# Performance work log

Measured on AMD Instinct MI355X. Metric: run time of the kernel, lower is better.

## Reference

```python
import jax, jax.numpy as jnp
import numpy as np

N, E = 50000, 800000
IN_D, HID, H1, OUT_D, H2, EDGE_D = 64, 16, 8, 64, 2, 1
NEG_SLOPE = 0.2


def gatv2_layer(x, src, dst, edge_attr, Wl, Wr, We, att, bias, concat):
    """PyG GATv2Conv (add_self_loops=False, share_weights=False), eval mode (no dropout)."""
    n = x.shape[0]
    H, C = att.shape
    xl = (x @ Wl).reshape(n, H, C)            # source transform
    xr = (x @ Wr).reshape(n, H, C)            # target transform
    ee = (edge_attr @ We).reshape(-1, H, C)   # edge embedding
    z = jax.nn.leaky_relu(xl[src] + xr[dst] + ee, NEG_SLOPE)  # [E,H,C]
    score = jnp.einsum('ehc,hc->eh', z, att)                  # [E,H]
    # softmax over incoming edges per target node
    m = jax.ops.segment_max(score, dst, num_segments=n)
    m = jnp.where(jnp.isfinite(m), m, 0.0)
    a = jnp.exp(score - m[dst])
    denom = jax.ops.segment_sum(a, dst, num_segments=n)
    alpha = a / (denom[dst] + 1e-16)                          # [E,H]
    msg = xl[src] * alpha[..., None]                          # [E,H,C]
    out = jax.ops.segment_sum(msg, dst, num_segments=n)       # [N,H,C]
    if concat:
        return out.reshape(n, H * C) + bias
    return out.mean(axis=1) + bias


def layer_norm(x, g, b):
    mu = x.mean(-1, keepdims=True)
    var = ((x - mu) ** 2).mean(-1, keepdims=True)
    return (x - mu) * jax.lax.rsqrt(var + 1e-5) * g + b


def setup_inputs() -> dict:
    key = jax.random.key(0)
    ks = jax.random.split(key, 24)
    def w(k, *shape):
        fan_in = shape[0]
        return jax.random.normal(k, shape, dtype=jnp.float32) * (1.0 / np.sqrt(fan_in))
    inp = {
        'x': jax.random.normal(ks[0], (N, IN_D), dtype=jnp.float32),
        'edge_index': jax.random.randint(ks[1], (2, E), 0, N, dtype=jnp.int64),
        'edge_attr': jax.random.normal(ks[2], (E, EDGE_D), dtype=jnp.float32),
        # layer 1 (heads=8, out=16, concat)
        'w1_l': w(ks[3], IN_D, H1 * HID), 'w1_r': w(ks[4], IN_D, H1 * HID),
        'w1_e': w(ks[5], EDGE_D, H1 * HID),
        'att1': jax.random.normal(ks[6], (H1, HID), dtype=jnp.float32) * 0.1,
        'b1': jnp.zeros((H1 * HID,), dtype=jnp.float32),
        # layer 2 (heads=2, out=64, mean)
        'w2_l': w(ks[7], H1 * HID, H2 * OUT_D), 'w2_r': w(ks[8], H1 * HID, H2 * OUT_D),
        'w2_e': w(ks[9], EDGE_D, H2 * OUT_D),
        'att2': jax.random.normal(ks[10], (H2, OUT_D), dtype=jnp.float32) * 0.1,
        'b2': jnp.zeros((OUT_D,), dtype=jnp.float32),
        # classifier: Linear + LayerNorm + GELU + ResidualBlockv2
        'wc': w(ks[11], OUT_D, OUT_D), 'bc': jnp.zeros((OUT_D,), dtype=jnp.float32),
        'ln_g': jnp.ones((OUT_D,), dtype=jnp.float32), 'ln_b': jnp.zeros((OUT_D,), dtype=jnp.float32),
        'wr': w(ks[12], OUT_D, OUT_D), 'br': jnp.zeros((OUT_D,), dtype=jnp.float32),
        'lnr_g': jnp.ones((OUT_D,), dtype=jnp.float32), 'lnr_b': jnp.zeros((OUT_D,), dtype=jnp.float32),
    }
    return inp


def reference(x, edge_index, edge_attr, w1_l, w1_r, w1_e, att1, b1,
              w2_l, w2_r, w2_e, att2, b2, wc, bc, ln_g, ln_b, wr, br, lnr_g, lnr_b):
    src, dst = edge_index[0], edge_index[1]
    h = jax.nn.relu(gatv2_layer(x, src, dst, edge_attr, w1_l, w1_r, w1_e, att1, b1, True))
    h = jax.nn.relu(gatv2_layer(h, src, dst, edge_attr, w2_l, w2_r, w2_e, att2, b2, False))
    h = jax.nn.gelu(layer_norm(h @ wc + bc, ln_g, ln_b), approximate=False)
    # ResidualBlockv2: Linear -> LayerNorm -> GELU with residual skip
    h = h + jax.nn.gelu(layer_norm(h @ wr + br, lnr_g, lnr_b), approximate=False)
    return h
```

## Files before the change

### kernel.cpp

```cpp
#include <hip/hip_runtime.h>
#include <math.h>

#define NNODE 50000
#define NEDGE 800000
#define NBLK 196

__device__ __forceinline__ float wsum64(float v) {
    #pragma unroll
    for (int m = 32; m >= 1; m >>= 1) v += __shfl_xor(v, m, 64);
    return v;
}

__device__ __forceinline__ float gelu_exact(float x) {
    return 0.5f * x * (1.0f + erff(x * 0.70710678118654752f));
}

__device__ __forceinline__ float lrelu(float z) { return z > 0.f ? z : 0.2f * z; }

__global__ void fill_u32(unsigned* __restrict__ p, unsigned v, int n) {
    int i = blockIdx.x * blockDim.x + threadIdx.x;
    if (i < n) p[i] = v;
}

__global__ __launch_bounds__(256) void build_deg(const int* __restrict__ ei, int* __restrict__ deg) {
    int e = blockIdx.x * 256 + threadIdx.x;
    if (e >= NEDGE) return;
    atomicAdd(&deg[ei[NEDGE + e]], 1);
}

__global__ __launch_bounds__(256) void scan1(const int* __restrict__ deg,
                                             int* __restrict__ partial,
                                             int* __restrict__ bsum) {
    __shared__ int tmp[256];
    int t = threadIdx.x;
    int gid = blockIdx.x * 256 + t;
    int v = (gid < NNODE) ? deg[gid] : 0;
    tmp[t] = v;
    __syncthreads();
    #pragma unroll
    for (int off = 1; off < 256; off <<= 1) {
        int u = (t >= off) ? tmp[t - off] : 0;
        __syncthreads();
        tmp[t] += u;
        __syncthreads();
    }
    if (gid < NNODE) partial[gid] = tmp[t] - v;
    if (t == 255) bsum[blockIdx.x] = tmp[255];
}

__global__ __launch_bounds__(256) void scan2(int* __restrict__ bsum, int* __restrict__ boff) {
    __shared__ int tmp[256];
    int t = threadIdx.x;
    int v = (t < NBLK) ? bsum[t] : 0;
    tmp[t] = v;
    __syncthreads();
    #pragma unroll
    for (int off = 1; off < 256; off <<= 1) {
        int u = (t >= off) ? tmp[t - off] : 0;
        __syncthreads();
        tmp[t] += u;
        __syncthreads();
    }
    if (t < NBLK) boff[t] = tmp[t] - v;
}

__global__ __launch_bounds__(256) void scan3(const int* __restrict__ partial,
                                             const int* __restrict__ boff,
                                             int* __restrict__ base,
                                             int* __restrict__ cursor) {
    int gid = blockIdx.x * 256 + threadIdx.x;
    if (gid < NNODE) {
        int b = partial[gid] + boff[blockIdx.x];
        base[gid] = b;
        cursor[gid] = b;
    }
    if (gid == 0) base[NNODE] = NEDGE;
}

__global__ __launch_bounds__(256) void scatter_edges(const int* __restrict__ ei,
                                                     const float* __restrict__ ea,
                                                     int* __restrict__ cursor,
                                                     int2* __restrict__ se) {
    int e = blockIdx.x * 256 + threadIdx.x;
    if (e >= NEDGE) return;
    int d = ei[NEDGE + e];
    int i = atomicAdd(&cursor[d], 1);
    se[i] = make_int2(ei[e], __float_as_int(ea[e]));
}

template<int K>
__global__ __launch_bounds__(256) void node_xform(const float* __restrict__ in,
                                                  const float* __restrict__ wl,
                                                  const float* __restrict__ wr,
                                                  float* __restrict__ xl,
                                                  float* __restrict__ xr) {
    __shared__ float xrow[32][K];
    int t = threadIdx.x;
    int n0 = blockIdx.x * 32;
    for (int idx = t; idx < 32 * (K / 4); idx += 256) {
        int row = idx / (K / 4), c4 = idx % (K / 4);
        float4 v = make_float4(0.f, 0.f, 0.f, 0.f);
        if (n0 + row < NNODE) v = ((const float4*)(in + (size_t)(n0 + row) * K))[c4];
        ((float4*)xrow[row])[c4] = v;
    }
    __syncthreads();
    int cg = t & 63, ns = t >> 6;
    const float* wsel = (cg < 32) ? wl : wr;
    float* osel = (cg < 32) ? xl : xr;
    int ccol = (cg & 31) * 4;
    const float* wp = wsel + ccol;
    const float* xbase = xrow[ns * 8];
    float4 acc[8];
    #pragma unroll
    for (int k = 0; k < 8; ++k) acc[k] = make_float4(0.f, 0.f, 0.f, 0.f);
    for (int i = 0; i < K; i += 4) {
        float4 w0 = *(const float4*)(wp + (size_t)(i + 0) * 128);
        float4 w1 = *(const float4*)(wp + (size_t)(i + 1) * 128);
        float4 w2 = *(const float4*)(wp + (size_t)(i + 2) * 128);
        float4 w3 = *(const float4*)(wp + (size_t)(i + 3) * 128);
        #pragma unroll
        for (int k = 0; k < 8; ++k) {
            float4 xv = *(const float4*)(xbase + (size_t)k * K + i);
            acc[k].x += xv.x * w0.x + xv.y * w1.x + xv.z * w2.x + xv.w * w3.x;
            acc[k].y += xv.x * w0.y + xv.y * w1.y + xv.z * w2.y + xv.w * w3.y;
            acc[k].z += xv.x * w0.z + xv.y * w1.z + xv.z * w2.z + xv.w * w3.z;
            acc[k].w += xv.x * w0.w + xv.y * w1.w + xv.z * w2.w + xv.w * w3.w;
        }
    }
    #pragma unroll
    for (int k = 0; k < 8; ++k) {
        int n = n0 + ns * 8 + k;
        if (n < NNODE) *(float4*)(osel + (size_t)n * 128 + ccol) = acc[k];
    }
}

__global__ __launch_bounds__(256) void fused1(const int* __restrict__ base,
                                              const int2* __restrict__ se,
                                              const float* __restrict__ xl,
                                              const float* __restrict__ xr,
                                              const float* __restrict__ w1e,
                                              const float* __restrict__ att1,
                                              const float* __restrict__ b1,
                                              float* __restrict__ h1) {
    int t = threadIdx.x;
    int wv = t >> 6, ln = t & 63;
    int half = ln >> 5, sub = ln & 31;
    int n = blockIdx.x * 4 + wv;
    int ch = sub * 4;
    float4 xrv = *(const float4*)(xr + (size_t)n * 128 + ch);
    float4 wev = *(const float4*)(w1e + ch);
    float4 atv = *(const float4*)(att1 + ch);
    int i0 = base[n], i1 = base[n + 1];
    float m = -1e30f, den = 0.f;
    float4 o = make_float4(0.f, 0.f, 0.f, 0.f);
    int i = i0 + half;
    if (i < i1) {
        int2 r = se[i];
        float4 xv = *(const float4*)(xl + (size_t)r.x * 128 + ch);
        float a = __int_as_float(r.y);
        for (i += 2; i < i1; i += 2) {
            int2 rn = se[i];
            float4 nxv = *(const float4*)(xl + (size_t)rn.x * 128 + ch);
            float na = __int_as_float(rn.y);
            float part = lrelu(fmaf(a, wev.x, xv.x + xrv.x)) * atv.x
                       + lrelu(fmaf(a, wev.y, xv.y + xrv.y)) * atv.y
                       + lrelu(fmaf(a, wev.z, xv.z + xrv.z)) * atv.z
                       + lrelu(fmaf(a, wev.w, xv.w + xrv.w)) * atv.w;
            part += __shfl_xor(part, 1, 64);
            part += __shfl_xor(part, 2, 64);
            float mn = fmaxf(m, part);
            float sc = __expf(m - mn);
            float p  = __expf(part - mn);
            den = den * sc + p;
            o.x = o.x * sc + p * xv.x;
            o.y = o.y * sc + p * xv.y;
            o.z = o.z * sc + p * xv.z;
            o.w = o.w * sc + p * xv.w;
            m = mn;
            xv = nxv; a = na;
        }
        float part = lrelu(fmaf(a, wev.x, xv.x + xrv.x)) * atv.x
                   + lrelu(fmaf(a, wev.y, xv.y + xrv.y)) * atv.y
                   + lrelu(fmaf(a, wev.z, xv.z + xrv.z)) * atv.z
                   + lrelu(fmaf(a, wev.w, xv.w + xrv.w)) * atv.w;
        part += __shfl_xor(part, 1, 64);
        part += __shfl_xor(part, 2, 64);
        float mn = fmaxf(m, part);
        float sc = __expf(m - mn);
        float p  = __expf(part - mn);
        den = den * sc + p;
        o.x = o.x * sc + p * xv.x;
        o.y = o.y * sc + p * xv.y;
        o.z = o.z * sc + p * xv.z;
        o.w = o.w * sc + p * xv.w;
        m = mn;
    }
    float m2   = __shfl_xor(m, 32, 64);
    float den2 = __shfl_xor(den, 32, 64);
    float4 o2;
    o2.x = __shfl_xor(o.x, 32, 64);
    o2.y = __shfl_xor(o.y, 32, 64);
    o2.z = __shfl_xor(o.z, 32, 64);
    o2.w = __shfl_xor(o.w, 32, 64);
    float mn = fmaxf(m, m2);
    float s1 = __expf(m - mn), s2 = __expf(m2 - mn);
    den = den * s1 + den2 * s2;
    float inv = 1.f / (den + 1e-16f);
    if (half == 0) {
        float4 bv = *(const float4*)(b1 + ch);
        float4 res;
        res.x = fmaxf((o.x * s1 + o2.x * s2) * inv + bv.x, 0.f);
        res.y = fmaxf((o.y * s1 + o2.y * s2) * inv + bv.y, 0.f);
        res.z = fmaxf((o.z * s1 + o2.z * s2) * inv + bv.z, 0.f);
        res.w = fmaxf((o.w * s1 + o2.w * s2) * inv + bv.w, 0.f);
        *(float4*)(h1 + (size_t)n * 128 + ch) = res;
    }
}

__global__ __launch_bounds__(256) void fused2cls(const int* __restrict__ base,
                                                 const int2* __restrict__ se,
                                                 const float* __restrict__ xl,
                                                 const float* __restrict__ xr,
                                                 const float* __restrict__ w2e,
                                                 const float* __restrict__ att2,
                                                 const float* __restrict__ b2,
                                                 const float* __restrict__ wc,
                                                 const float* __restrict__ bc,
                                                 const float* __restrict__ lng,
                                                 const float* __restrict__ lnb,
                                                 const float* __restrict__ wrr,
                                                 const float* __restrict__ brr,
                                                 const float* __restrict__ lrg,
                                                 const float* __restrict__ lrb,
                                                 float* __restrict__ out) {
    __shared__ float rowH[4][64];
    __shared__ float rowB[4][64];
    int t = threadIdx.x;
    int wv = t >> 6, ln = t & 63;
    int half = ln >> 5, sub = ln & 31;
    int n = blockIdx.x * 4 + wv;
    int ch = sub * 4;
    float4 xrv = *(const float4*)(xr + (size_t)n * 128 + ch);
    float4 wev = *(const float4*)(w2e + ch);
    float4 atv = *(const float4*)(att2 + ch);
    int i0 = base[n], i1 = base[n + 1];
    float m = -1e30f, den = 0.f;
    float4 o = make_float4(0.f, 0.f, 0.f, 0.f);
    int i = i0 + half;
    if (i < i1) {
        int2 r = se[i];
        float4 xv = *(const float4*)(xl + (size_t)r.x * 128 + ch);
        float a = __int_as_float(r.y);
        for (i += 2; i < i1; i += 2) {
            int2 rn = se[i];
            float4 nxv = *(const float4*)(xl + (size_t)rn.x * 128 + ch);
            float na = __int_as_float(rn.y);
            float part = lrelu(fmaf(a, wev.x, xv.x + xrv.x)) * atv.x
                       + lrelu(fmaf(a, wev.y, xv.y + xrv.y)) * atv.y
                       + lrelu(fmaf(a, wev.z, xv.z + xrv.z)) * atv.z
                       + lrelu(fmaf(a, wev.w, xv.w + xrv.w)) * atv.w;
            part += __shfl_xor(part, 1, 64);
            part += __shfl_xor(part, 2, 64);
            part += __shfl_xor(part, 4, 64);
            part += __shfl_xor(part, 8, 64);
            float mn = fmaxf(m, part);
            float sc = __expf(m - mn);
            float p  = __expf(part - mn);
            den = den * sc + p;
            o.x = o.x * sc + p * xv.x;
            o.y = o.y * sc + p * xv.y;
            o.z = o.z * sc + p * xv.z;
            o.w = o.w * sc + p * xv.w;
            m = mn;
            xv = nxv; a = na;
        }
        float part = lrelu(fmaf(a, wev.x, xv.x + xrv.x)) * atv.x
                   + lrelu(fmaf(a, wev.y, xv.y + xrv.y)) * atv.y
                   + lrelu(fmaf(a, wev.z, xv.z + xrv.z)) * atv.z
                   + lrelu(fmaf(a, wev.w, xv.w + xrv.w)) * atv.w;
        part += __shfl_xor(part, 1, 64);
        part += __shfl_xor(part, 2, 64);
        part += __shfl_xor(part, 4, 64);
        part += __shfl_xor(part, 8, 64);
        float mn = fmaxf(m, part);
        float sc = __expf(m - mn);
        float p  = __expf(part - mn);
        den = den * sc + p;
        o.x = o.x * sc + p * xv.x;
        o.y = o.y * sc + p * xv.y;
        o.z = o.z * sc + p * xv.z;
        o.w = o.w * sc + p * xv.w;
        m = mn;
    }
    float m2   = __shfl_xor(m, 32, 64);
    float den2 = __shfl_xor(den, 32, 64);
    float4 o2;
    o2.x = __shfl_xor(o.x, 32, 64);
    o2.y = __shfl_xor(o.y, 32, 64);
    o2.z = __shfl_xor(o.z, 32, 64);
    o2.w = __shfl_xor(o.w, 32, 64);
    float mn = fmaxf(m, m2);
    float s1 = __expf(m - mn), s2 = __expf(m2 - mn);
    den = den * s1 + den2 * s2;
    float inv = 1.f / (den + 1e-16f);
    float4 v;
    v.x = (o.x * s1 + o2.x * s2) * inv;
    v.y = (o.y * s1 + o2.y * s2) * inv;
    v.z = (o.z * s1 + o2.z * s2) * inv;
    v.w = (o.w * s1 + o2.w * s2) * inv;
    float4 u;
    u.x = __shfl_xor(v.x, 16, 64);
    u.y = __shfl_xor(v.y, 16, 64);
    u.z = __shfl_xor(v.z, 16, 64);
    u.w = __shfl_xor(v.w, 16, 64);
    if (half == 0 && sub < 16) {
        float4 bv = *(const float4*)(b2 + ch);
        float4 res;
        res.x = fmaxf(0.5f * (v.x + u.x) + bv.x, 0.f);
        res.y = fmaxf(0.5f * (v.y + u.y) + bv.y, 0.f);
        res.z = fmaxf(0.5f * (v.z + u.z) + bv.z, 0.f);
        res.w = fmaxf(0.5f * (v.w + u.w) + bv.w, 0.f);
        *(float4*)(&rowH[wv][ch]) = res;
    }
    __syncthreads();
    float acc = bc[ln];
    #pragma unroll 8
    for (int j = 0; j < 64; ++j) acc += rowH[wv][j] * wc[j * 64 + ln];
    float mu = wsum64(acc) * (1.f / 64.f);
    float dv = acc - mu;
    float var = wsum64(dv * dv) * (1.f / 64.f);
    float y = dv * rsqrtf(var + 1e-5f) * lng[ln] + lnb[ln];
    float g1 = gelu_exact(y);
    rowB[wv][ln] = g1;
    __syncthreads();
    float acc2 = brr[ln];
    #pragma unroll 8
    for (int j = 0; j < 64; ++j) acc2 += rowB[wv][j] * wrr[j * 64 + ln];
    float mu2 = wsum64(acc2) * (1.f / 64.f);
    float dv2 = acc2 - mu2;
    float var2 = wsum64(dv2 * dv2) * (1.f / 64.f);
    float y2 = dv2 * rsqrtf(var2 + 1e-5f) * lrg[ln] + lrb[ln];
    float g2 = gelu_exact(y2);
    out[(size_t)n * 64 + ln] = g1 + g2;
}

extern "C" void kernel_launch(void* const* d_in, const int* in_sizes, int n_in,
                              void* d_out, int out_size, void* d_ws, size_t ws_size,
                              hipStream_t stream) {
    const float* x    = (const float*)d_in[0];
    const int*   ei   = (const int*)d_in[1];
    const float* ea   = (const float*)d_in[2];
    const float* w1l  = (const float*)d_in[3];
    const float* w1r  = (const float*)d_in[4];
    const float* w1e  = (const float*)d_in[5];
    const float* att1 = (const float*)d_in[6];
    const float* b1   = (const float*)d_in[7];
    const float* w2l  = (const float*)d_in[8];
    const float* w2r  = (const float*)d_in[9];
    const float* w2e  = (const float*)d_in[10];
    const float* att2 = (const float*)d_in[11];
    const float* b2   = (const float*)d_in[12];
    const float* wc   = (const float*)d_in[13];
    const float* bc   = (const float*)d_in[14];
    const float* lng  = (const float*)d_in[15];
    const float* lnb  = (const float*)d_in[16];
    const float* wr   = (const float*)d_in[17];
    const float* br   = (const float*)d_in[18];
    const float* lrg  = (const float*)d_in[19];
    const float* lrb  = (const float*)d_in[20];

    float* ws = (float*)d_ws;
    const size_t N128 = (size_t)NNODE * 128;
    float* xl = ws;
    float* xr = xl + N128;
    float* h1 = xr + N128;
    int2*  se      = (int2*)(h1 + N128);
    int*   deg     = (int*)(se + NEDGE);
    int*   partial = deg + NNODE;
    int*   base    = partial + NNODE;
    int*   cursor  = base + NNODE + 1;
    int*   bsum    = cursor + NNODE;
    int*   boff    = bsum + 256;

    const int EB  = NEDGE / 256;
    const int NBX = (NNODE + 31) / 32;
    const int NB4 = NNODE / 4;

    fill_u32<<<NBLK, 256, 0, stream>>>((unsigned*)deg, 0u, NNODE);
    build_deg<<<EB, 256, 0, stream>>>(ei, deg);
    scan1<<<NBLK, 256, 0, stream>>>(deg, partial, bsum);
    scan2<<<1, 256, 0, stream>>>(bsum, boff);
    scan3<<<NBLK, 256, 0, stream>>>(partial, boff, base, cursor);
    scatter_edges<<<EB, 256, 0, stream>>>(ei, ea, cursor, se);

    node_xform<64><<<NBX, 256, 0, stream>>>(x, w1l, w1r, xl, xr);
    fused1<<<NB4, 256, 0, stream>>>(base, se, xl, xr, w1e, att1, b1, h1);

    node_xform<128><<<NBX, 256, 0, stream>>>(h1, w2l, w2r, xl, xr);
    fused2cls<<<NB4, 256, 0, stream>>>(base, se, xl, xr, w2e, att2, b2,
                                       wc, bc, lng, lnb, wr, br, lrg, lrb,
                                       (float*)d_out);
}
```

Baseline: 340.8 us.

## Split classifier out of layer-2 aggregation and cache weights in LDS

Layer-2 attention aggregation now writes its output to a workspace buffer, and the classifier MLP (two linear layers with LayerNorm and GELU) runs as a separate kernel. The new classifier kernel stages both 64x64 weight matrices and the bias/norm vectors in shared memory. Each wave processes four nodes in sequence to amortize that staging. This aims to keep weight reads off global memory and make the aggregation kernel lighter. In exchange it adds an extra launch, an intermediate global round trip, and large LDS usage that limits occupancy.

```diff
diff --git a/kernel.cpp b/kernel.cpp
--- a/kernel.cpp
+++ b/kernel.cpp
@@ -217,24 +217,14 @@
     }
 }
 
-__global__ __launch_bounds__(256) void fused2cls(const int* __restrict__ base,
-                                                 const int2* __restrict__ se,
-                                                 const float* __restrict__ xl,
-                                                 const float* __restrict__ xr,
-                                                 const float* __restrict__ w2e,
-                                                 const float* __restrict__ att2,
-                                                 const float* __restrict__ b2,
-                                                 const float* __restrict__ wc,
-                                                 const float* __restrict__ bc,
-                                                 const float* __restrict__ lng,
-                                                 const float* __restrict__ lnb,
-                                                 const float* __restrict__ wrr,
-                                                 const float* __restrict__ brr,
-                                                 const float* __restrict__ lrg,
-                                                 const float* __restrict__ lrb,
-                                                 float* __restrict__ out) {
-    __shared__ float rowH[4][64];
-    __shared__ float rowB[4][64];
+__global__ __launch_bounds__(256) void fused2(const int* __restrict__ base,
+                                              const int2* __restrict__ se,
+                                              const float* __restrict__ xl,
+                                              const float* __restrict__ xr,
+                                              const float* __restrict__ w2e,
+                                              const float* __restrict__ att2,
+                                              const float* __restrict__ b2,
+                                              float* __restrict__ h2) {
     int t = threadIdx.x;
     int wv = t >> 6, ln = t & 63;
     int half = ln >> 5, sub = ln & 31;
@@ -320,28 +310,68 @@
         res.y = fmaxf(0.5f * (v.y + u.y) + bv.y, 0.f);
         res.z = fmaxf(0.5f * (v.z + u.z) + bv.z, 0.f);
         res.w = fmaxf(0.5f * (v.w + u.w) + bv.w, 0.f);
-        *(float4*)(&rowH[wv][ch]) = res;
+        *(float4*)(h2 + (size_t)n * 64 + ch) = res;
+    }
+}
+
+__global__ __launch_bounds__(256) void classifier(const float* __restrict__ h2,
+                                                  const float* __restrict__ wc,
+                                                  const float* __restrict__ bc,
+                                                  const float* __restrict__ lng,
+                                                  const float* __restrict__ lnb,
+                                                  const float* __restrict__ wrr,
+                                                  const float* __restrict__ brr,
+                                                  const float* __restrict__ lrg,
+                                                  const float* __restrict__ lrb,
+                                                  float* __restrict__ out) {
+    __shared__ float swc[4096];
+    __shared__ float swr[4096];
+    __shared__ float svec[384];
+    __shared__ float rowA[4][64];
+    __shared__ float rowB[4][64];
+    int t = threadIdx.x;
+    for (int i = t; i < 4096; i += 256) { swc[i] = wc[i]; swr[i] = wrr[i]; }
+    if (t < 64) {
+        svec[t]       = bc[t];
+        svec[64 + t]  = lng[t];
+        svec[128 + t] = lnb[t];
+        svec[192 + t] = brr[t];
+        svec[256 + t] = lrg[t];
+        svec[320 + t] = lrb[t];
     }
     __syncthreads();
-    float acc = bc[ln];
-    #pragma unroll 8
-    for (int j = 0; j < 64; ++j) acc += rowH[wv][j] * wc[j * 64 + ln];
-    float mu = wsum64(acc) * (1.f / 64.f);
-    float dv = acc - mu;
-    float var = wsum64(dv * dv) * (1.f / 64.f);
-    float y = dv * rsqrtf(var + 1e-5f) * lng[ln] + lnb[ln];
-    float g1 = gelu_exact(y);
-    rowB[wv][ln] = g1;
-    __syncthreads();
-    float acc2 = brr[ln];
-    #pragma unroll 8
-    for (int j = 0; j < 64; ++j) acc2 += rowB[wv][j] * wrr[j * 64 + ln];
-    float mu2 = wsum64(acc2) * (1.f / 64.f);
-    float dv2 = acc2 - mu2;
-    float var2 = wsum64(dv2 * dv2) * (1.f / 64.f);
-    float y2 = dv2 * rsqrtf(var2 + 1e-5f) * lrg[ln] + lrb[ln];
-    float g2 = gelu_exact(y2);
-    out[(size_t)n * 64 + ln] = g1 + g2;
+    int wv = t >> 6, ln = t & 63;
+    #pragma unroll
+    for (int k = 0; k < 4; ++k) {
+        int n = blockIdx.x * 16 + wv * 4 + k;
+        rowA[wv][ln] = h2[(size_t)n * 64 + ln];
+        float acc = svec[ln];
+        #pragma unroll 4
+        for (int j = 0; j < 64; j += 4) {
+            float4 hv = *(const float4*)&rowA[wv][j];
+            acc += hv.x * swc[(j + 0) * 64 + ln] + hv.y * swc[(j + 1) * 64 + ln]
+                 + hv.z * swc[(j + 2) * 64 + ln] + hv.w * swc[(j + 3) * 64 + ln];
+        }
+        float mu = wsum64(acc) * (1.f / 64.f);
+        float dv = acc - mu;
+        float var = wsum64(dv * dv) * (1.f / 64.f);
+        float y = dv * rsqrtf(var + 1e-5f) * svec[64 + ln] + svec[128 + ln];
+        float g1 = gelu_exact(y);
+        rowB[wv][ln] = g1;
+        float acc2 = svec[192 + ln];
+        #pragma unroll 4
+        for (int j = 0; j < 64; j += 4) {
+            float4 hv = *(const float4*)&rowB[wv][j];
+            acc2 += hv.x * swr[(j + 0) * 64 + ln] + hv.y * swr[(j + 1) * 64 + ln]
+                  + hv.z * swr[(j + 2) * 64 + ln] + hv.w * swr[(j + 3) * 64 + ln];
+        }
+        float mu2 = wsum64(acc2) * (1.f / 64.f);
+        float dv2 = acc2 - mu2;
+        float var2 = wsum64(dv2 * dv2) * (1.f / 64.f);
+        float y2 = dv2 * rsqrtf(var2 + 1e-5f) * svec[256 + ln] + svec[320 + ln];
+        float g2 = gelu_exact(y2);
+        out[(size_t)n * 64 + ln] = g1 + g2;
+    }
 }
 
 extern "C" void kernel_launch(void* const* d_in, const int* in_sizes, int n_in,
@@ -374,7 +404,8 @@
     float* xl = ws;
     float* xr = xl + N128;
     float* h1 = xr + N128;
-    int2*  se      = (int2*)(h1 + N128);
+    float* h2 = h1 + N128;
+    int2*  se      = (int2*)(h2 + (size_t)NNODE * 64);
     int*   deg     = (int*)(se + NEDGE);
     int*   partial = deg + NNODE;
     int*   base    = partial + NNODE;
@@ -397,7 +428,8 @@
     fused1<<<NB4, 256, 0, stream>>>(base, se, xl, xr, w1e, att1, b1, h1);
 
     node_xform<128><<<NBX, 256, 0, stream>>>(h1, w2l, w2r, xl, xr);
-    fused2cls<<<NB4, 256, 0, stream>>>(base, se, xl, xr, w2e, att2, b2,
-                                       wc, bc, lng, lnb, wr, br, lrg, lrb,
-                                       (float*)d_out);
-}
+    fused2<<<NB4, 256, 0, stream>>>(base, se, xl, xr, w2e, att2, b2, h2);
+
+    classifier<<<NNODE / 16, 256, 0, stream>>>(h2, wc, bc, lng, lnb, wr, br, lrg, lrb,
+                                               (float*)d_out);
+}
```

Result: slower. 352.6 us (+3.5%).
